# Performance work log

Measured on AMD Instinct MI355X. Metric: run time of the kernel, lower is better.

## Reference

```python
import jax, jax.numpy as jnp
import numpy as np


def setup_inputs() -> dict:
    key = jax.random.key(0)
    k0, k1, k2, k3, k4 = jax.random.split(key, 5)
    B, d_inner, L, d_state = 64, 384, 197, 16
    x = jax.random.normal(k0, (B, d_inner, L), dtype=jnp.float32)
    # deltaA = exp(delta*A) lies in (0,1); uniform keeps the recurrence stable
    deltaA = jax.random.uniform(k1, (B, d_inner, L, d_state), dtype=jnp.float32)
    deltaB = jax.random.normal(k2, (B, d_inner, L, d_state), dtype=jnp.float32)
    C = jax.random.normal(k3, (B, d_state, L), dtype=jnp.float32)
    D = jax.random.normal(k4, (d_inner,), dtype=jnp.float32)
    return {"x": x, "deltaA": deltaA, "deltaB": deltaB, "C": C, "D": D}


def reference(x, deltaA, deltaB, C, D):
    """Selective scan: h_t = deltaB_t*x_t + deltaA_t*h_{t-1}; y_t = h_t @ C_t.
    x:(B,d,L) deltaA/deltaB:(B,d,L,n) C:(B,n,L) D:(d,)
    """
    deltaB_x = deltaB * x[..., None]              # (B,d,L,n)
    dA_t = jnp.moveaxis(deltaA, 2, 0)             # (L,B,d,n)
    dBx_t = jnp.moveaxis(deltaB_x, 2, 0)          # (L,B,d,n)
    C_t = jnp.moveaxis(C, 2, 0)                   # (L,B,n)

    def step(h, inputs):
        a, bx, c = inputs
        h = bx + a * h                            # (B,d,n)
        y = jnp.einsum("bdn,bn->bd", h, c)        # (B,d)
        return h, y

    h0 = jnp.zeros(dA_t.shape[1:], dtype=x.dtype)
    _, ys = jax.lax.scan(step, h0, (dA_t, dBx_t, C_t))  # ys: (L,B,d)
    y = jnp.moveaxis(ys, 0, 2)                    # (B,d,L)
    return y + x * D[:, None]
```

## Files before the change

### kernel.cpp

```cpp
#include <hip/hip_runtime.h>


#define B_   64
#define DIN  384
#define L_   197
#define N_   16
#define GROUPS_PER_BLOCK 16

__global__ __launch_bounds__(256)
void ssm_scan_kernel(const float* __restrict__ x,
                     const float* __restrict__ dA,
                     const float* __restrict__ dB,
                     const float* __restrict__ C,
                     const float* __restrict__ D,
                     float* __restrict__ y)
{
    __shared__ float Cs[N_ * L_];

    const int tid = threadIdx.x;
    const int b   = blockIdx.y;

    const float* Cg = C + (size_t)b * (N_ * L_);
    for (int i = tid; i < N_ * L_; i += 256) Cs[i] = Cg[i];
    __syncthreads();

    const int grp = tid >> 4;
    const int n   = tid & 15;
    const int d   = blockIdx.x * GROUPS_PER_BLOCK + grp;

    const size_t bd = (size_t)b * DIN + d;
    const float* pA = dA + bd * (size_t)(L_ * N_) + n;
    const float* pB = dB + bd * (size_t)(L_ * N_) + n;
    const float* px = x  + bd * L_;
    float*       py = y  + bd * L_;
    const float  Dd = D[d];
    const float* Cn = Cs + n * L_;

    float h = 0.0f;
    int t = 0;

    for (; t + 4 <= L_; t += 4) {
        const float a0 = pA[(t+0)*N_], a1 = pA[(t+1)*N_];
        const float a2 = pA[(t+2)*N_], a3 = pA[(t+3)*N_];
        const float g0 = pB[(t+0)*N_], g1 = pB[(t+1)*N_];
        const float g2 = pB[(t+2)*N_], g3 = pB[(t+3)*N_];
        const float x0 = px[t+0], x1 = px[t+1], x2 = px[t+2], x3 = px[t+3];
        const float c0 = Cn[t+0], c1 = Cn[t+1], c2 = Cn[t+2], c3 = Cn[t+3];

        h = fmaf(a0, h, g0 * x0);  float p0 = h * c0;
        h = fmaf(a1, h, g1 * x1);  float p1 = h * c1;
        h = fmaf(a2, h, g2 * x2);  float p2 = h * c2;
        h = fmaf(a3, h, g3 * x3);  float p3 = h * c3;

        #pragma unroll
        for (int m = 1; m < 16; m <<= 1) {
            p0 += __shfl_xor(p0, m);
            p1 += __shfl_xor(p1, m);
            p2 += __shfl_xor(p2, m);
            p3 += __shfl_xor(p3, m);
        }

        if (n == 0) {
            py[t+0] = fmaf(x0, Dd, p0);
            py[t+1] = fmaf(x1, Dd, p1);
            py[t+2] = fmaf(x2, Dd, p2);
            py[t+3] = fmaf(x3, Dd, p3);
        }
    }

    for (; t < L_; ++t) {
        const float a  = pA[t*N_];
        const float g  = pB[t*N_];
        const float xv = px[t];
        h = fmaf(a, h, g * xv);
        float p = h * Cn[t];
        #pragma unroll
        for (int m = 1; m < 16; m <<= 1) p += __shfl_xor(p, m);
        if (n == 0) py[t] = fmaf(xv, Dd, p);
    }
}

extern "C" void kernel_launch(void* const* d_in, const int* in_sizes, int n_in,
                              void* d_out, int out_size, void* d_ws, size_t ws_size,
                              hipStream_t stream) {
    const float* x  = (const float*)d_in[0];
    const float* dA = (const float*)d_in[1];
    const float* dB = (const float*)d_in[2];
    const float* C  = (const float*)d_in[3];
    const float* D  = (const float*)d_in[4];
    float* y = (float*)d_out;

    dim3 grid(DIN / GROUPS_PER_BLOCK, B_);
    dim3 block(256);
    ssm_scan_kernel<<<grid, block, 0, stream>>>(x, dA, dB, C, D, y);
}
```

Baseline: 162.8 us.

## Vectorize state dimension per thread with float4 loads and transposed C

Each thread now owns four state elements and loads them as float4, so a d-channel uses 4 lanes instead of 16. The shuffle reduction shrinks from four to two stages. C is transposed in shared memory so it can be read as float4. Output stores are spread across lanes. The kernel runs 128-thread blocks with 32 channels each, which gives fewer total threads and less latency hiding for this memory-bound scan.

```diff
diff --git a/kernel.cpp b/kernel.cpp
--- a/kernel.cpp
+++ b/kernel.cpp
@@ -5,78 +5,104 @@
 #define DIN  384
 #define L_   197
 #define N_   16
-#define GROUPS_PER_BLOCK 16
+#define GRP_PER_BLOCK 32
 
-__global__ __launch_bounds__(256)
-void ssm_scan_kernel(const float* __restrict__ x,
-                     const float* __restrict__ dA,
-                     const float* __restrict__ dB,
-                     const float* __restrict__ C,
-                     const float* __restrict__ D,
-                     float* __restrict__ y)
+__global__ __launch_bounds__(128)
+void ssm_scan4(const float* __restrict__ x,
+               const float* __restrict__ dA,
+               const float* __restrict__ dB,
+               const float* __restrict__ C,
+               const float* __restrict__ D,
+               float* __restrict__ y)
 {
-    __shared__ float Cs[N_ * L_];
+    __shared__ float Cs[L_ * N_];
 
     const int tid = threadIdx.x;
     const int b   = blockIdx.y;
 
     const float* Cg = C + (size_t)b * (N_ * L_);
-    for (int i = tid; i < N_ * L_; i += 256) Cs[i] = Cg[i];
+    for (int i = tid; i < N_ * L_; i += 128) {
+        const int n = i / L_;
+        const int t = i - n * L_;
+        Cs[t * N_ + n] = Cg[i];
+    }
     __syncthreads();
 
-    const int grp = tid >> 4;
-    const int n   = tid & 15;
-    const int d   = blockIdx.x * GROUPS_PER_BLOCK + grp;
+    const int grp = tid >> 2;
+    const int n4  = tid & 3;
+    const int d   = blockIdx.x * GRP_PER_BLOCK + grp;
 
     const size_t bd = (size_t)b * DIN + d;
-    const float* pA = dA + bd * (size_t)(L_ * N_) + n;
-    const float* pB = dB + bd * (size_t)(L_ * N_) + n;
-    const float* px = x  + bd * L_;
-    float*       py = y  + bd * L_;
-    const float  Dd = D[d];
-    const float* Cn = Cs + n * L_;
+    const float4* pA = (const float4*)dA + bd * (size_t)(L_ * 4) + n4;
+    const float4* pB = (const float4*)dB + bd * (size_t)(L_ * 4) + n4;
+    const float*  px = x + bd * L_;
+    float*        py = y + bd * L_;
+    const float   Dd = D[d];
 
-    float h = 0.0f;
+    float h0 = 0.f, h1 = 0.f, h2 = 0.f, h3 = 0.f;
     int t = 0;
 
     for (; t + 4 <= L_; t += 4) {
-        const float a0 = pA[(t+0)*N_], a1 = pA[(t+1)*N_];
-        const float a2 = pA[(t+2)*N_], a3 = pA[(t+3)*N_];
-        const float g0 = pB[(t+0)*N_], g1 = pB[(t+1)*N_];
-        const float g2 = pB[(t+2)*N_], g3 = pB[(t+3)*N_];
-        const float x0 = px[t+0], x1 = px[t+1], x2 = px[t+2], x3 = px[t+3];
-        const float c0 = Cn[t+0], c1 = Cn[t+1], c2 = Cn[t+2], c3 = Cn[t+3];
+        const float4 a0 = pA[(t+0)*4], a1 = pA[(t+1)*4];
+        const float4 a2 = pA[(t+2)*4], a3 = pA[(t+3)*4];
+        const float4 g0 = pB[(t+0)*4], g1 = pB[(t+1)*4];
+        const float4 g2 = pB[(t+2)*4], g3 = pB[(t+3)*4];
+        const float  x0 = px[t+0], x1 = px[t+1], x2 = px[t+2], x3 = px[t+3];
+        const float4 c0 = *(const float4*)(Cs + (t+0)*N_ + n4*4);
+        const float4 c1 = *(const float4*)(Cs + (t+1)*N_ + n4*4);
+        const float4 c2 = *(const float4*)(Cs + (t+2)*N_ + n4*4);
+        const float4 c3 = *(const float4*)(Cs + (t+3)*N_ + n4*4);
 
-        h = fmaf(a0, h, g0 * x0);  float p0 = h * c0;
-        h = fmaf(a1, h, g1 * x1);  float p1 = h * c1;
-        h = fmaf(a2, h, g2 * x2);  float p2 = h * c2;
-        h = fmaf(a3, h, g3 * x3);  float p3 = h * c3;
+        h0 = fmaf(a0.x, h0, g0.x * x0);
+        h1 = fmaf(a0.y, h1, g0.y * x0);
+        h2 = fmaf(a0.z, h2, g0.z * x0);
+        h3 = fmaf(a0.w, h3, g0.w * x0);
+        float p0 = fmaf(h0, c0.x, fmaf(h1, c0.y, fmaf(h2, c0.z, h3 * c0.w)));
 
-        #pragma unroll
-        for (int m = 1; m < 16; m <<= 1) {
-            p0 += __shfl_xor(p0, m);
-            p1 += __shfl_xor(p1, m);
-            p2 += __shfl_xor(p2, m);
-            p3 += __shfl_xor(p3, m);
-        }
+        h0 = fmaf(a1.x, h0, g1.x * x1);
+        h1 = fmaf(a1.y, h1, g1.y * x1);
+        h2 = fmaf(a1.z, h2, g1.z * x1);
+        h3 = fmaf(a1.w, h3, g1.w * x1);
+        float p1 = fmaf(h0, c1.x, fmaf(h1, c1.y, fmaf(h2, c1.z, h3 * c1.w)));
 
-        if (n == 0) {
-            py[t+0] = fmaf(x0, Dd, p0);
-            py[t+1] = fmaf(x1, Dd, p1);
-            py[t+2] = fmaf(x2, Dd, p2);
-            py[t+3] = fmaf(x3, Dd, p3);
-        }
+        h0 = fmaf(a2.x, h0, g2.x * x2);
+        h1 = fmaf(a2.y, h1, g2.y * x2);
+        h2 = fmaf(a2.z, h2, g2.z * x2);
+        h3 = fmaf(a2.w, h3, g2.w * x2);
+        float p2 = fmaf(h0, c2.x, fmaf(h1, c2.y, fmaf(h2, c2.z, h3 * c2.w)));
+
+        h0 = fmaf(a3.x, h0, g3.x * x3);
+        h1 = fmaf(a3.y, h1, g3.y * x3);
+        h2 = fmaf(a3.z, h2, g3.z * x3);
+        h3 = fmaf(a3.w, h3, g3.w * x3);
+        float p3 = fmaf(h0, c3.x, fmaf(h1, c3.y, fmaf(h2, c3.z, h3 * c3.w)));
+
+        p0 += __shfl_xor(p0, 1);  p0 += __shfl_xor(p0, 2);
+        p1 += __shfl_xor(p1, 1);  p1 += __shfl_xor(p1, 2);
+        p2 += __shfl_xor(p2, 1);  p2 += __shfl_xor(p2, 2);
+        p3 += __shfl_xor(p3, 1);  p3 += __shfl_xor(p3, 2);
+
+        const float y0 = fmaf(x0, Dd, p0);
+        const float y1 = fmaf(x1, Dd, p1);
+        const float y2 = fmaf(x2, Dd, p2);
+        const float y3 = fmaf(x3, Dd, p3);
+        float yv = (n4 == 0) ? y0 : (n4 == 1) ? y1 : (n4 == 2) ? y2 : y3;
+        py[t + n4] = yv;
     }
 
     for (; t < L_; ++t) {
-        const float a  = pA[t*N_];
-        const float g  = pB[t*N_];
-        const float xv = px[t];
-        h = fmaf(a, h, g * xv);
-        float p = h * Cn[t];
-        #pragma unroll
-        for (int m = 1; m < 16; m <<= 1) p += __shfl_xor(p, m);
-        if (n == 0) py[t] = fmaf(xv, Dd, p);
+        const float4 a = pA[t*4];
+        const float4 g = pB[t*4];
+        const float  xv = px[t];
+        const float4 c = *(const float4*)(Cs + t*N_ + n4*4);
+        h0 = fmaf(a.x, h0, g.x * xv);
+        h1 = fmaf(a.y, h1, g.y * xv);
+        h2 = fmaf(a.z, h2, g.z * xv);
+        h3 = fmaf(a.w, h3, g.w * xv);
+        float p = fmaf(h0, c.x, fmaf(h1, c.y, fmaf(h2, c.z, h3 * c.w)));
+        p += __shfl_xor(p, 1);
+        p += __shfl_xor(p, 2);
+        if (n4 == 0) py[t] = fmaf(xv, Dd, p);
     }
 }
 
@@ -90,7 +116,7 @@
     const float* D  = (const float*)d_in[4];
     float* y = (float*)d_out;
 
-    dim3 grid(DIN / GROUPS_PER_BLOCK, B_);
-    dim3 block(256);
-    ssm_scan_kernel<<<grid, block, 0, stream>>>(x, dA, dB, C, D, y);
+    dim3 grid(DIN / GRP_PER_BLOCK, B_);
+    dim3 block(128);
+    ssm_scan4<<<grid, block, 0, stream>>>(x, dA, dB, C, D, y);
 }
```

Result: faster. 156.9 us (-3.6%).

## Software-pipeline scan loads, stage x in LDS, and use DPP reductions

Applied to the files above, without the earlier changes.

Restructures the scan loop so the dA/dB values for the next 8 timesteps are loaded into registers while the current 8 are computed, with sched_barriers to hold that overlap in place. The x rows are staged into shared memory, the first two butterfly reduction steps use DPP instead of shuffles, and the 8 outputs are written by 8 lanes at once rather than one lane per step. The intent is to hide global memory latency on the serial recurrence and cut reduction and store overhead. The cost is higher register pressure under launch bounds of 8 blocks per CU, and more LDS per block.

```diff
diff --git a/kernel.cpp b/kernel.cpp
--- a/kernel.cpp
+++ b/kernel.cpp
@@ -5,79 +5,101 @@
 #define DIN  384
 #define L_   197
 #define N_   16
-#define GROUPS_PER_BLOCK 16
+#define NB   24
 
-__global__ __launch_bounds__(256)
-void ssm_scan_kernel(const float* __restrict__ x,
-                     const float* __restrict__ dA,
-                     const float* __restrict__ dB,
-                     const float* __restrict__ C,
-                     const float* __restrict__ D,
-                     float* __restrict__ y)
+#define DPPADD(p, C) do { \
+    int _r = __builtin_amdgcn_update_dpp(0, __float_as_int(p), (C), 0xF, 0xF, true); \
+    (p) += __int_as_float(_r); } while (0)
+
+__global__ __launch_bounds__(256, 8)
+void ssm_scan16(const float* __restrict__ x, const float* __restrict__ dA,
+                const float* __restrict__ dB, const float* __restrict__ C,
+                const float* __restrict__ D, float* __restrict__ y)
 {
     __shared__ float Cs[N_ * L_];
+    __shared__ float Xs[16 * L_];
 
     const int tid = threadIdx.x;
     const int b   = blockIdx.y;
+    const int d0  = blockIdx.x * 16;
 
     const float* Cg = C + (size_t)b * (N_ * L_);
     for (int i = tid; i < N_ * L_; i += 256) Cs[i] = Cg[i];
+    const float* Xg = x + ((size_t)b * DIN + d0) * L_;
+    for (int i = tid; i < 16 * L_; i += 256) Xs[i] = Xg[i];
     __syncthreads();
 
-    const int grp = tid >> 4;
-    const int n   = tid & 15;
-    const int d   = blockIdx.x * GROUPS_PER_BLOCK + grp;
+    const int g = tid >> 4;
+    const int n = tid & 15;
+    const size_t bd = (size_t)b * DIN + d0 + g;
 
-    const size_t bd = (size_t)b * DIN + d;
     const float* pA = dA + bd * (size_t)(L_ * N_) + n;
-    const float* pB = dB + bd * (size_t)(L_ * N_) + n;
-    const float* px = x  + bd * L_;
-    float*       py = y  + bd * L_;
-    const float  Dd = D[d];
-    const float* Cn = Cs + n * L_;
+    const float* pG = dB + bd * (size_t)(L_ * N_) + n;
+    float*      pyL = y + bd * L_;
+    const float  Dd = D[d0 + g];
+    const float* CsL = Cs + n * L_;
+    const float* XsL = Xs + g * L_;
 
-    float h = 0.0f;
-    int t = 0;
+    float h = 0.f;
 
-    for (; t + 4 <= L_; t += 4) {
-        const float a0 = pA[(t+0)*N_], a1 = pA[(t+1)*N_];
-        const float a2 = pA[(t+2)*N_], a3 = pA[(t+3)*N_];
-        const float g0 = pB[(t+0)*N_], g1 = pB[(t+1)*N_];
-        const float g2 = pB[(t+2)*N_], g3 = pB[(t+3)*N_];
-        const float x0 = px[t+0], x1 = px[t+1], x2 = px[t+2], x3 = px[t+3];
-        const float c0 = Cn[t+0], c1 = Cn[t+1], c2 = Cn[t+2], c3 = Cn[t+3];
+    float PA0,PA1,PA2,PA3,PA4,PA5,PA6,PA7, PG0,PG1,PG2,PG3,PG4,PG5,PG6,PG7;
+    float QA0,QA1,QA2,QA3,QA4,QA5,QA6,QA7, QG0,QG1,QG2,QG3,QG4,QG5,QG6,QG7;
 
-        h = fmaf(a0, h, g0 * x0);  float p0 = h * c0;
-        h = fmaf(a1, h, g1 * x1);  float p1 = h * c1;
-        h = fmaf(a2, h, g2 * x2);  float p2 = h * c2;
-        h = fmaf(a3, h, g3 * x3);  float p3 = h * c3;
+#define LOADB(Pa, Pg, t0) do { \
+    Pa##0=pA[((t0)+0)*N_]; Pa##1=pA[((t0)+1)*N_]; Pa##2=pA[((t0)+2)*N_]; Pa##3=pA[((t0)+3)*N_]; \
+    Pa##4=pA[((t0)+4)*N_]; Pa##5=pA[((t0)+5)*N_]; Pa##6=pA[((t0)+6)*N_]; Pa##7=pA[((t0)+7)*N_]; \
+    Pg##0=pG[((t0)+0)*N_]; Pg##1=pG[((t0)+1)*N_]; Pg##2=pG[((t0)+2)*N_]; Pg##3=pG[((t0)+3)*N_]; \
+    Pg##4=pG[((t0)+4)*N_]; Pg##5=pG[((t0)+5)*N_]; Pg##6=pG[((t0)+6)*N_]; Pg##7=pG[((t0)+7)*N_]; \
+} while (0)
 
-        #pragma unroll
-        for (int m = 1; m < 16; m <<= 1) {
-            p0 += __shfl_xor(p0, m);
-            p1 += __shfl_xor(p1, m);
-            p2 += __shfl_xor(p2, m);
-            p3 += __shfl_xor(p3, m);
+#define ST(Pa, Pg, t0, j, yv) do { \
+    const float xv = XsL[(t0)+(j)]; \
+    h = fmaf(Pa##j, h, Pg##j * xv); \
+    float p = h * CsL[(t0)+(j)]; \
+    DPPADD(p, 0xB1);    \
+    DPPADD(p, 0x4E);    \
+    p += __shfl_xor(p, 4); \
+    p += __shfl_xor(p, 8); \
+    yv = fmaf(xv, Dd, p); \
+} while (0)
+
+#define BODY(Pa, Pg, t0) do { \
+    float y0,y1,y2,y3,y4,y5,y6,y7; \
+    ST(Pa,Pg,t0,0,y0); ST(Pa,Pg,t0,1,y1); ST(Pa,Pg,t0,2,y2); ST(Pa,Pg,t0,3,y3); \
+    ST(Pa,Pg,t0,4,y4); ST(Pa,Pg,t0,5,y5); ST(Pa,Pg,t0,6,y6); ST(Pa,Pg,t0,7,y7); \
+    const float v0=(n&1)?y1:y0, v1=(n&1)?y3:y2, v2=(n&1)?y5:y4, v3=(n&1)?y7:y6; \
+    const float w0=(n&2)?v1:v0, w1=(n&2)?v3:v2; \
+    if (n < 8) pyL[(t0) + n] = (n&4)?w1:w0; \
+} while (0)
+
+    LOADB(PA, PG, 0);
+    for (int k = 0; k < NB; k += 2) {
+        const int tq = (k + 1) * 8;
+        LOADB(QA, QG, tq);
+        __builtin_amdgcn_sched_barrier(0);
+        BODY(PA, PG, k * 8);
+        if (k + 2 < NB) {
+            LOADB(PA, PG, (k + 2) * 8);
+        } else {
+            PA0=pA[192*N_]; PA1=pA[193*N_]; PA2=pA[194*N_]; PA3=pA[195*N_]; PA4=pA[196*N_];
+            PG0=pG[192*N_]; PG1=pG[193*N_]; PG2=pG[194*N_]; PG3=pG[195*N_]; PG4=pG[196*N_];
         }
-
-        if (n == 0) {
-            py[t+0] = fmaf(x0, Dd, p0);
-            py[t+1] = fmaf(x1, Dd, p1);
-            py[t+2] = fmaf(x2, Dd, p2);
-            py[t+3] = fmaf(x3, Dd, p3);
-        }
+        __builtin_amdgcn_sched_barrier(0);
+        BODY(QA, QG, tq);
     }
 
-    for (; t < L_; ++t) {
-        const float a  = pA[t*N_];
-        const float g  = pB[t*N_];
-        const float xv = px[t];
-        h = fmaf(a, h, g * xv);
-        float p = h * Cn[t];
-        #pragma unroll
-        for (int m = 1; m < 16; m <<= 1) p += __shfl_xor(p, m);
-        if (n == 0) py[t] = fmaf(xv, Dd, p);
+    {
+        float y0,y1,y2,y3,y4;
+        ST(PA,PG,192,0,y0); ST(PA,PG,192,1,y1); ST(PA,PG,192,2,y2);
+        ST(PA,PG,192,3,y3); ST(PA,PG,192,4,y4);
+        const float v0=(n&1)?y1:y0, v1=(n&1)?y3:y2;
+        const float w0=(n&2)?v1:v0;
+        const float val=(n&4)?y4:w0;
+        if (n < 5) pyL[192 + n] = val;
     }
+#undef BODY
+#undef ST
+#undef LOADB
 }
 
 extern "C" void kernel_launch(void* const* d_in, const int* in_sizes, int n_in,
@@ -90,7 +112,7 @@
     const float* D  = (const float*)d_in[4];
     float* y = (float*)d_out;
 
-    dim3 grid(DIN / GROUPS_PER_BLOCK, B_);
+    dim3 grid(DIN / 16, B_);
     dim3 block(256);
-    ssm_scan_kernel<<<grid, block, 0, stream>>>(x, dA, dB, C, D, y);
+    ssm_scan16<<<grid, block, 0, stream>>>(x, dA, dB, C, D, y);
 }
```

New measurement: 146.7 us. 1.11x faster.

## Replace serial per-thread scan with chunked parallel scan using DPP and float4 loads

Applied to the files above, without the earlier changes.

Each 16-lane row now covers one d channel across 16 timesteps per chunk: each lane holds 4 timesteps by 4 states and loads them as float4. A local 4-step scan is followed by a DPP-based cross-lane associative scan with a carry broadcast through ds_swizzle, and the chunks are double-buffered in registers. C is transposed into padded shared memory so the C·h reduction is a float4 dot plus a 2-step DPP sum. This removes the long serial dependency chain and the strided scalar loads, at the cost of extra multiplies for the scan composition, higher register pressure, and complex tail handling.

```diff
diff --git a/kernel.cpp b/kernel.cpp
--- a/kernel.cpp
+++ b/kernel.cpp
@@ -5,79 +5,154 @@
 #define DIN  384
 #define L_   197
 #define N_   16
-#define GROUPS_PER_BLOCK 16
+#define CSTR 20
+#define NCH  12
 
-__global__ __launch_bounds__(256)
-void ssm_scan_kernel(const float* __restrict__ x,
-                     const float* __restrict__ dA,
-                     const float* __restrict__ dB,
-                     const float* __restrict__ C,
-                     const float* __restrict__ D,
-                     float* __restrict__ y)
+template<int CTRL>
+__device__ __forceinline__ float dppmov(float src, float oldv) {
+    return __int_as_float(__builtin_amdgcn_update_dpp(
+        __float_as_int(oldv), __float_as_int(src), CTRL, 0xF, 0xF, false));
+}
+__device__ __forceinline__ float qsum(float p) {
+    p += __int_as_float(__builtin_amdgcn_update_dpp(0, __float_as_int(p), 0xB1, 0xF, 0xF, true));
+    p += __int_as_float(__builtin_amdgcn_update_dpp(0, __float_as_int(p), 0x4E, 0xF, 0xF, true));
+    return p;
+}
+__device__ __forceinline__ float bcast12q(float v) {
+    return __int_as_float(__builtin_amdgcn_ds_swizzle(__float_as_int(v), 0x193));
+}
+
+__global__ __launch_bounds__(256, 2)
+void ssm_pscan(const float* __restrict__ x, const float* __restrict__ dA,
+               const float* __restrict__ dB, const float* __restrict__ C,
+               const float* __restrict__ D, float* __restrict__ y)
 {
-    __shared__ float Cs[N_ * L_];
+    __shared__ __align__(16) float Cs[L_ * CSTR];
 
     const int tid = threadIdx.x;
     const int b   = blockIdx.y;
 
     const float* Cg = C + (size_t)b * (N_ * L_);
-    for (int i = tid; i < N_ * L_; i += 256) Cs[i] = Cg[i];
+    for (int i = tid; i < N_ * L_; i += 256) {
+        const int n = i / L_;
+        const int t = i - n * L_;
+        Cs[t * CSTR + n] = Cg[i];
+    }
     __syncthreads();
 
-    const int grp = tid >> 4;
-    const int n   = tid & 15;
-    const int d   = blockIdx.x * GROUPS_PER_BLOCK + grp;
+    const int lane = tid & 63;
+    const int wav  = tid >> 6;
+    const int row  = lane >> 4;
+    const int p    = lane & 15;
+    const int p4   = p >> 2;
+    const int q    = p & 3;
 
+    const int d   = blockIdx.x * 16 + wav * 4 + row;
     const size_t bd = (size_t)b * DIN + d;
-    const float* pA = dA + bd * (size_t)(L_ * N_) + n;
-    const float* pB = dB + bd * (size_t)(L_ * N_) + n;
-    const float* px = x  + bd * L_;
-    float*       py = y  + bd * L_;
-    const float  Dd = D[d];
-    const float* Cn = Cs + n * L_;
 
-    float h = 0.0f;
-    int t = 0;
+    const float* Arow = dA + bd * (size_t)(L_ * N_);
+    const float* Brow = dB + bd * (size_t)(L_ * N_);
+    const float* Xrow = x  + bd * L_;
+    float*       Yrow = y  + bd * L_;
+    const float  Dd   = D[d];
+    const int laneAB  = p4 * 64 + q * 4;
+    const float* CsQ  = Cs + q * 4;
 
-    for (; t + 4 <= L_; t += 4) {
-        const float a0 = pA[(t+0)*N_], a1 = pA[(t+1)*N_];
-        const float a2 = pA[(t+2)*N_], a3 = pA[(t+3)*N_];
-        const float g0 = pB[(t+0)*N_], g1 = pB[(t+1)*N_];
-        const float g2 = pB[(t+2)*N_], g3 = pB[(t+3)*N_];
-        const float x0 = px[t+0], x1 = px[t+1], x2 = px[t+2], x3 = px[t+3];
-        const float c0 = Cn[t+0], c1 = Cn[t+1], c2 = Cn[t+2], c3 = Cn[t+3];
+    float hcx = 0.f, hcy = 0.f, hcz = 0.f, hcw = 0.f;
 
-        h = fmaf(a0, h, g0 * x0);  float p0 = h * c0;
-        h = fmaf(a1, h, g1 * x1);  float p1 = h * c1;
-        h = fmaf(a2, h, g2 * x2);  float p2 = h * c2;
-        h = fmaf(a3, h, g3 * x3);  float p3 = h * c3;
+    float4 PA0,PA1,PA2,PA3, PB0,PB1,PB2,PB3;
+    float4 QA0,QA1,QA2,QA3, QB0,QB1,QB2,QB3;
+    float  Px0,Px1,Px2,Px3, Qx0,Qx1,Qx2,Qx3;
 
-        #pragma unroll
-        for (int m = 1; m < 16; m <<= 1) {
-            p0 += __shfl_xor(p0, m);
-            p1 += __shfl_xor(p1, m);
-            p2 += __shfl_xor(p2, m);
-            p3 += __shfl_xor(p3, m);
-        }
+#define LOADC(Pfx, c) do { \
+    const float* _a = Arow + (c)*256 + laneAB; \
+    const float* _g = Brow + (c)*256 + laneAB; \
+    Pfx##A0 = *(const float4*)(_a +  0); Pfx##A1 = *(const float4*)(_a + 16); \
+    Pfx##A2 = *(const float4*)(_a + 32); Pfx##A3 = *(const float4*)(_a + 48); \
+    Pfx##B0 = *(const float4*)(_g +  0); Pfx##B1 = *(const float4*)(_g + 16); \
+    Pfx##B2 = *(const float4*)(_g + 32); Pfx##B3 = *(const float4*)(_g + 48); \
+    const float* _x = Xrow + (c)*16 + p4*4; \
+    Pfx##x0 = _x[0]; Pfx##x1 = _x[1]; Pfx##x2 = _x[2]; Pfx##x3 = _x[3]; \
+} while (0)
 
-        if (n == 0) {
-            py[t+0] = fmaf(x0, Dd, p0);
-            py[t+1] = fmaf(x1, Dd, p1);
-            py[t+2] = fmaf(x2, Dd, p2);
-            py[t+3] = fmaf(x3, Dd, p3);
-        }
+#define LOADT(Pfx) do { \
+    const int _tb = 192 + p4*4; \
+    const int _t0 = _tb   > 196 ? 196 : _tb; \
+    const int _t1 = _tb+1 > 196 ? 196 : _tb+1; \
+    const int _t2 = _tb+2 > 196 ? 196 : _tb+2; \
+    const int _t3 = _tb+3 > 196 ? 196 : _tb+3; \
+    Pfx##A0 = *(const float4*)(Arow + _t0*16 + q*4); \
+    Pfx##A1 = *(const float4*)(Arow + _t1*16 + q*4); \
+    Pfx##A2 = *(const float4*)(Arow + _t2*16 + q*4); \
+    Pfx##A3 = *(const float4*)(Arow + _t3*16 + q*4); \
+    Pfx##B0 = *(const float4*)(Brow + _t0*16 + q*4); \
+    Pfx##B1 = *(const float4*)(Brow + _t1*16 + q*4); \
+    Pfx##B2 = *(const float4*)(Brow + _t2*16 + q*4); \
+    Pfx##B3 = *(const float4*)(Brow + _t3*16 + q*4); \
+    Pfx##x0 = Xrow[_t0]; Pfx##x1 = Xrow[_t1]; \
+    Pfx##x2 = Xrow[_t2]; Pfx##x3 = Xrow[_t3]; \
+} while (0)
+
+#define SCANE(Pfx, E) do { \
+    Pfx##B0.E *= Pfx##x0; Pfx##B1.E *= Pfx##x1; \
+    Pfx##B2.E *= Pfx##x2; Pfx##B3.E *= Pfx##x3; \
+    Pfx##B1.E = fmaf(Pfx##A1.E, Pfx##B0.E, Pfx##B1.E); Pfx##A1.E *= Pfx##A0.E; \
+    Pfx##B2.E = fmaf(Pfx##A2.E, Pfx##B1.E, Pfx##B2.E); Pfx##A2.E *= Pfx##A1.E; \
+    Pfx##B3.E = fmaf(Pfx##A3.E, Pfx##B2.E, Pfx##B3.E); Pfx##A3.E *= Pfx##A2.E; \
+    float _ta = Pfx##A3.E, _tv = Pfx##B3.E; \
+    { float _pa = dppmov<0x114>(_ta, 1.0f), _pb = dppmov<0x114>(_tv, 0.0f); \
+      _tv = fmaf(_ta, _pb, _tv); _ta *= _pa; } \
+    { float _pa = dppmov<0x118>(_ta, 1.0f), _pb = dppmov<0x118>(_tv, 0.0f); \
+      _tv = fmaf(_ta, _pb, _tv); _ta *= _pa; } \
+    const float _Ea = dppmov<0x114>(_ta, 1.0f); \
+    const float _Eb = dppmov<0x114>(_tv, 0.0f); \
+    const float _s  = fmaf(_Ea, hc##E, _Eb); \
+    Pfx##B0.E = fmaf(Pfx##A0.E, _s, Pfx##B0.E); \
+    Pfx##B1.E = fmaf(Pfx##A1.E, _s, Pfx##B1.E); \
+    Pfx##B2.E = fmaf(Pfx##A2.E, _s, Pfx##B2.E); \
+    Pfx##B3.E = fmaf(Pfx##A3.E, _s, Pfx##B3.E); \
+} while (0)
+
+#define YJ(Pfx, j, tcj, yf) do { \
+    const float4 _c4 = *(const float4*)(CsQ + (tcj)*CSTR); \
+    float _yp = fmaf(Pfx##B##j.x, _c4.x, fmaf(Pfx##B##j.y, _c4.y, \
+                 fmaf(Pfx##B##j.z, _c4.z, Pfx##B##j.w * _c4.w))); \
+    _yp = qsum(_yp); \
+    yf = fmaf(Pfx##x##j, Dd, _yp); \
+} while (0)
+
+#define COMPUTE(Pfx, c, TAIL) do { \
+    SCANE(Pfx, x); SCANE(Pfx, y); SCANE(Pfx, z); SCANE(Pfx, w); \
+    const int _t0s = (TAIL) ? (192 + p4*4) : ((c)*16 + p4*4); \
+    int _c0 = _t0s, _c1 = _t0s+1, _c2 = _t0s+2, _c3 = _t0s+3; \
+    if (TAIL) { _c0 = _c0>196?196:_c0; _c1 = _c1>196?196:_c1; \
+                _c2 = _c2>196?196:_c2; _c3 = _c3>196?196:_c3; } \
+    float _yf0,_yf1,_yf2,_yf3; \
+    YJ(Pfx, 0, _c0, _yf0); YJ(Pfx, 1, _c1, _yf1); \
+    YJ(Pfx, 2, _c2, _yf2); YJ(Pfx, 3, _c3, _yf3); \
+    hcx = bcast12q(Pfx##B3.x); hcy = bcast12q(Pfx##B3.y); \
+    hcz = bcast12q(Pfx##B3.z); hcw = bcast12q(Pfx##B3.w); \
+    const float _ys = (q==0) ? _yf0 : (q==1) ? _yf1 : (q==2) ? _yf2 : _yf3; \
+    if (!(TAIL) || p4 == 0 || (p4 == 1 && q == 0)) Yrow[_t0s + q] = _ys; \
+} while (0)
+
+    LOADC(P, 0);
+#pragma unroll 1
+    for (int c = 0; c < NCH; c += 2) {
+        LOADC(Q, c + 1);
+        __builtin_amdgcn_sched_barrier(0);
+        COMPUTE(P, c, 0);
+        if (c + 2 < NCH) { LOADC(P, c + 2); } else { LOADT(P); }
+        __builtin_amdgcn_sched_barrier(0);
+        COMPUTE(Q, c + 1, 0);
     }
+    COMPUTE(P, 0, 1);
 
-    for (; t < L_; ++t) {
-        const float a  = pA[t*N_];
-        const float g  = pB[t*N_];
-        const float xv = px[t];
-        h = fmaf(a, h, g * xv);
-        float p = h * Cn[t];
-        #pragma unroll
-        for (int m = 1; m < 16; m <<= 1) p += __shfl_xor(p, m);
-        if (n == 0) py[t] = fmaf(xv, Dd, p);
-    }
+#undef COMPUTE
+#undef YJ
+#undef SCANE
+#undef LOADT
+#undef LOADC
 }
 
 extern "C" void kernel_launch(void* const* d_in, const int* in_sizes, int n_in,
@@ -88,9 +163,9 @@
     const float* dB = (const float*)d_in[2];
     const float* C  = (const float*)d_in[3];
     const float* D  = (const float*)d_in[4];
-    float* y = (float*)d_out;
+    float* yo = (float*)d_out;
 
-    dim3 grid(DIN / GROUPS_PER_BLOCK, B_);
+    dim3 grid(DIN / 16, B_);
     dim3 block(256);
-    ssm_scan_kernel<<<grid, block, 0, stream>>>(x, dA, dB, C, D, y);
+    ssm_pscan<<<grid, block, 0, stream>>>(x, dA, dB, C, D, yo);
 }
```

After: 155.1 us. 4.7% less time.
